# Optimization experiments

Hardware: AMD Instinct MI355X
Metric: run time of the kernel (lower is better)

The kernel has to match this reference:

```python
import jax, jax.numpy as jnp
import numpy as np

V, H, E = 32000, 512, 256
B, NC, LSC, LCM, LIS = 64, 10, 128, 64, 32


def _lstm_last(x, Wih, Whh, b):
    # x: [N, T, E] -> final (h, c) each [N, H]. PyTorch gate order i, f, g, o.
    N = x.shape[0]
    Hd = Whh.shape[1]
    h0 = jnp.zeros((N, Hd), x.dtype)

    def step(carry, xt):
        h, c = carry
        z = xt @ Wih.T + h @ Whh.T + b  # [N, 4H]
        i, f, g, o = jnp.split(z, 4, axis=-1)
        c = jax.nn.sigmoid(f) * c + jax.nn.sigmoid(i) * jnp.tanh(g)
        h = jax.nn.sigmoid(o) * jnp.tanh(c)
        return (h, c), None

    (h, c), _ = jax.lax.scan(step, (h0, h0), jnp.swapaxes(x, 0, 1))
    return h, c


def setup_inputs() -> dict:
    key = jax.random.key(0)
    ks = jax.random.split(key, 24)
    s = 0.02
    inp = {
        'comments': jax.random.randint(ks[0], (B, NC, LSC), 0, V),
        'cm': jax.random.randint(ks[1], (B, NC, LCM), 0, V),
        'issue': jax.random.randint(ks[2], (B, LIS), 0, V),
        'emb_sc': jax.random.normal(ks[3], (V, E), jnp.float32) * s,
        'emb_cm': jax.random.normal(ks[4], (V, E), jnp.float32) * s,
        'emb_is': jax.random.normal(ks[5], (V, E), jnp.float32) * s,
        'Wih_sc': jax.random.normal(ks[6], (4 * H, E), jnp.float32) * s,
        'Whh_sc': jax.random.normal(ks[7], (4 * H, H), jnp.float32) * s,
        'b_sc': jnp.zeros((4 * H,), jnp.float32),
        'Wih_cm': jax.random.normal(ks[8], (4 * H, E), jnp.float32) * s,
        'Whh_cm': jax.random.normal(ks[9], (4 * H, H), jnp.float32) * s,
        'b_cm': jnp.zeros((4 * H,), jnp.float32),
        'Wih_is': jax.random.normal(ks[10], (4 * H, E), jnp.float32) * s,
        'Whh_is': jax.random.normal(ks[11], (4 * H, H), jnp.float32) * s,
        'b_is': jnp.zeros((4 * H,), jnp.float32),
        'Wmh': jax.random.normal(ks[12], (1, 2 * H), jnp.float32) * s,
        'bmh': jnp.zeros((1,), jnp.float32),
        'Wmc': jax.random.normal(ks[13], (1, 2 * H), jnp.float32) * s,
        'bmc': jnp.zeros((1,), jnp.float32),
        'Wfh': jax.random.normal(ks[14], (H, NC + H), jnp.float32) * s,
        'bfh': jnp.zeros((H,), jnp.float32),
        'Wfc': jax.random.normal(ks[15], (H, NC + H), jnp.float32) * s,
        'bfc': jnp.zeros((H,), jnp.float32),
    }
    return inp


def reference(comments, cm, issue, emb_sc, emb_cm, emb_is,
              Wih_sc, Whh_sc, b_sc, Wih_cm, Whh_cm, b_cm,
              Wih_is, Whh_is, b_is, Wmh, bmh, Wmc, bmc,
              Wfh, bfh, Wfc, bfc):
    Bb, Nc, Lsc = comments.shape
    sc_ids = comments.reshape(Bb * Nc, Lsc)
    cm_ids = cm.reshape(Bb * Nc, cm.shape[-1])
    # embed + LSTM over all B*NC commit sequences at once (batched ragged loop)
    h_sc, c_sc = _lstm_last(emb_sc[sc_ids], Wih_sc, Whh_sc, b_sc)
    h_cm, c_cm = _lstm_last(emb_cm[cm_ids], Wih_cm, Whh_cm, b_cm)
    hcat = jnp.concatenate([h_sc, h_cm], axis=-1)  # [B*NC, 2H]
    ccat = jnp.concatenate([c_sc, c_cm], axis=-1)
    hm = (hcat @ Wmh.T + bmh).reshape(Bb, Nc)  # per-commit scalar merge
    cmm = (ccat @ Wmc.T + bmc).reshape(Bb, Nc)
    h_is, c_is = _lstm_last(emb_is[issue], Wih_is, Whh_is, b_is)  # [B, H]
    h = jnp.concatenate([hm, h_is], axis=-1) @ Wfh.T + bfh  # [B, H]
    c = jnp.concatenate([cmm, c_is], axis=-1) @ Wfc.T + bfc
    # torch code cats per-PR (1,1,H) states along dim=1 -> (1, B, H)
    return h[None], c[None]
```

## Files before the change

### kernel.cpp

```cpp
#include <hip/hip_runtime.h>
#include <math.h>

#define E 256
#define Hh 512

typedef __attribute__((ext_vector_type(8))) short short8;
typedef __attribute__((ext_vector_type(4))) float f32x4;
typedef __attribute__((ext_vector_type(4))) unsigned uint4v;


struct LstmP {
  const int* ids;
  const float* emb;
  const unsigned short* Wih;
  const unsigned short* Whh;
  const float* bias;
  unsigned short* h0;
  float* c;
  int T;
  int nh;
};

__device__ unsigned g_cnt[42*32];

__device__ __forceinline__ float bf2f(unsigned short x){
  union { unsigned u; float f; } v; v.u = ((unsigned)x) << 16; return v.f;
}
__device__ __forceinline__ unsigned short f2bf(float f){
  union { float f; unsigned u; } v; v.f = f;
  unsigned u = v.u;
  return (unsigned short)((u + 0x7fffu + ((u >> 16) & 1u)) >> 16);
}
__device__ __forceinline__ short8 cvt8(const float* p){
  f32x4 x = *(const f32x4*)p;
  f32x4 y = *(const f32x4*)(p + 4);
  short8 r;
  r[0]=(short)f2bf(x[0]); r[1]=(short)f2bf(x[1]); r[2]=(short)f2bf(x[2]); r[3]=(short)f2bf(x[3]);
  r[4]=(short)f2bf(y[0]); r[5]=(short)f2bf(y[1]); r[6]=(short)f2bf(y[2]); r[7]=(short)f2bf(y[3]);
  return r;
}
__device__ __forceinline__ float sigm(float x){
  return __builtin_amdgcn_rcpf(1.0f + __builtin_amdgcn_exp2f(-1.44269504f*x));
}
__device__ __forceinline__ float tanh_f(float x){
  return 1.0f - 2.0f*__builtin_amdgcn_rcpf(1.0f + __builtin_amdgcn_exp2f(2.88539008f*x));
}

__global__ void zero_ws_kernel(uint4* p, int n){
  int i = blockIdx.x*256 + threadIdx.x;
  if (i < n){ uint4 z; z.x=0u; z.y=0u; z.z=0u; z.w=0u; p[i]=z; }
}

__global__ void zero_cnt_kernel(){
  for (int i = threadIdx.x; i < 42*32; i += 256) g_cnt[i] = 0u;
}

__global__ __launch_bounds__(256) void cvt_kernel(const float* src, unsigned short* dst, int n8){
  int i = blockIdx.x*256 + threadIdx.x;
  if (i < n8){
    *(short8*)(dst + (size_t)i*8) = cvt8(src + (size_t)i*8);
  }
}

__global__ __launch_bounds__(256, 2) void lstm_persist(LstmP sc, LstmP cm, LstmP is_)
{
  __shared__ unsigned short hs[32][512];
  __shared__ unsigned short sh_h[32][72];

  LstmP P; int tile, grp;
  {
    int idx = blockIdx.x;
    if (idx < 160){ P = sc;  tile = idx;        grp = tile >> 3; }
    else if (idx < 320){ P = cm;  tile = idx - 160;  grp = 20 + (tile >> 3); }
    else { P = is_; tile = idx - 320;  grp = 40 + (tile >> 3); }
  }
  const int tid  = threadIdx.x;
  const int w    = tid >> 6;
  const int lane = tid & 63;
  const int l15  = lane & 15;
  const int q    = lane >> 4;
  const int mb = tile >> 3, jt = tile & 7;
  const int m0 = mb*32, j0 = jt*64;
  const int jw = j0 + w*16;
  const int T = P.T;
  unsigned* cgp = &g_cnt[grp*32];
  const int xr = (l15 & 7) << 3;

  const int* idrow[2];
  #pragma unroll
  for (int mi=0; mi<2; ++mi){
    int m = m0 + mi*16 + l15;
    idrow[mi] = P.ids + (size_t)m*T;
  }
  const unsigned short* bg1[4];
  const unsigned short* bg2[4];
  float bvv[4];
  #pragma unroll
  for (int g=0; g<4; ++g){
    int n = g*Hh + jw + l15;
    bg1[g] = P.Wih + (size_t)n*E  + q*8;
    bg2[g] = P.Whh + (size_t)n*Hh + q*8;
    bvv[g] = P.bias[n];
  }

  float cc[8];
  #pragma unroll
  for (int i=0;i<8;++i) cc[i] = 0.f;

  for (int t = 0; t < T; ++t){
    const unsigned short* h_in  = P.h0 + (size_t)(t&1)*P.nh;
    unsigned short*       h_out = P.h0 + (size_t)((t+1)&1)*P.nh;

    f32x4 acc[2][4];
    #pragma unroll
    for (int i=0;i<2;++i)
      #pragma unroll
      for (int g=0;g<4;++g) acc[i][g] = (f32x4){0.f,0.f,0.f,0.f};

    uint4v stg[8];
    if (t > 0){
      if (tid == 0){
        unsigned tgt = 8u * (unsigned)t;
        long guard = 0;
        while (__hip_atomic_load(cgp, __ATOMIC_RELAXED, __HIP_MEMORY_SCOPE_AGENT) < tgt){
          __builtin_amdgcn_s_sleep(1);
          if (++guard > 2000000L) break;
        }
      }
      __syncthreads();
      asm volatile("" ::: "memory");

      const unsigned short* base = h_in + (size_t)m0*Hh;
      #pragma unroll
      for (int i=0;i<8;++i){
        int d = (tid + 256*i + (jt<<8)) & 2047;
        const void* ap = (const void*)(base + (size_t)d*8);
        asm volatile("global_load_dwordx4 %0, %1, off sc0 sc1"
                     : "=v"(stg[i]) : "v"(ap) : "memory");
      }
    }

    const float* ap1[2];
    #pragma unroll
    for (int mi=0; mi<2; ++mi){
      int id = idrow[mi][t];
      ap1[mi] = P.emb + (size_t)id*E + q*8;
    }
    #pragma unroll 2
    for (int kc=0; kc<8; ++kc){
      short8 a[2], b[4];
      #pragma unroll
      for (int mi=0;mi<2;++mi) a[mi] = cvt8(ap1[mi] + kc*32);
      #pragma unroll
      for (int g=0;g<4;++g) b[g] = *(const short8*)(bg1[g] + kc*32);
      #pragma unroll
      for (int mi=0;mi<2;++mi)
        #pragma unroll
        for (int g=0;g<4;++g)
          acc[mi][g] = __builtin_amdgcn_mfma_f32_16x16x32_bf16(a[mi], b[g], acc[mi][g], 0,0,0);
    }

    if (t > 0){
      asm volatile("s_waitcnt vmcnt(0)" ::: "memory");
      #pragma unroll
      for (int i=0;i<8;++i){
        int d = (tid + 256*i + (jt<<8)) & 2047;
        int row = d >> 6, cp = d & 63;
        *(uint4v*)&hs[row][(cp ^ (row & 7)) << 3] = stg[i];
      }
      __syncthreads();

      #pragma unroll 2
      for (int kc=0; kc<16; ++kc){
        short8 a[2], b[4];
        #pragma unroll
        for (int mi=0;mi<2;++mi)
          a[mi] = *(const short8*)&hs[mi*16 + l15][(kc*32 + q*8) ^ xr];
        #pragma unroll
        for (int g=0;g<4;++g) b[g] = *(const short8*)(bg2[g] + kc*32);
        #pragma unroll
        for (int mi=0;mi<2;++mi)
          #pragma unroll
          for (int g=0;g<4;++g)
            acc[mi][g] = __builtin_amdgcn_mfma_f32_16x16x32_bf16(a[mi], b[g], acc[mi][g], 0,0,0);
      }
    }

    #pragma unroll
    for (int mi=0;mi<2;++mi)
      #pragma unroll
      for (int r=0;r<4;++r){
        float zi = acc[mi][0][r] + bvv[0];
        float zf = acc[mi][1][r] + bvv[1];
        float zg = acc[mi][2][r] + bvv[2];
        float zo = acc[mi][3][r] + bvv[3];
        float cn = sigm(zf)*cc[mi*4+r] + sigm(zi)*tanh_f(zg);
        float hn = sigm(zo)*tanh_f(cn);
        cc[mi*4+r] = cn;
        sh_h[mi*16 + q*4 + r][w*16 + l15] = f2bf(hn);
      }
    __syncthreads();

    {
      int m = tid >> 3, oct = tid & 7;
      uint4v pk = *(const uint4v*)&sh_h[m][oct*8];
      void* ap = (void*)(h_out + (size_t)(m0+m)*Hh + j0 + oct*8);
      asm volatile("global_store_dwordx4 %0, %1, off sc0 sc1"
                   :: "v"(ap), "v"(pk) : "memory");
    }

    asm volatile("s_waitcnt vmcnt(0)" ::: "memory");
    __syncthreads();
    if (tid == 0)
      __hip_atomic_fetch_add(cgp, 1u, __ATOMIC_RELAXED, __HIP_MEMORY_SCOPE_AGENT);
  }

  #pragma unroll
  for (int mi=0;mi<2;++mi)
    #pragma unroll
    for (int r=0;r<4;++r)
      P.c[(size_t)(m0 + mi*16 + q*4 + r)*Hh + jw + l15] = cc[mi*4+r];
}

__global__ __launch_bounds__(256) void out_kernel(
    const unsigned short* hsc, const unsigned short* hcm, const unsigned short* his,
    const float* csc, const float* ccm, const float* cis,
    const float* Wmh, const float* bmh, const float* Wmc, const float* bmc,
    const float* Wfh, const float* bfh, const float* Wfc, const float* bfc,
    float* out)
{
  const int b    = blockIdx.x >> 2;
  const int kind = (blockIdx.x >> 1) & 1;
  const int half = blockIdx.x & 1;
  const int tid  = threadIdx.x;
  const int w = tid >> 6, lane = tid & 63;
  const float* Wm = kind ? Wmc : Wmh;
  const float* bm = kind ? bmc : bmh;
  const float* Wf = kind ? Wfc : Wfh;
  const float* bf = kind ? bfc : bfh;

  __shared__ float vis[512];
  __shared__ float wred[10][4];
  __shared__ float hmb[10];

  for (int k = tid; k < 512; k += 256)
    vis[k] = kind ? cis[(size_t)b*512 + k] : bf2f(his[(size_t)b*512 + k]);

  float pn[10];
  #pragma unroll
  for (int nc=0; nc<10; ++nc){
    size_t n = (size_t)b*10 + nc;
    float a = 0.f;
    #pragma unroll
    for (int kk=0; kk<2; ++kk){
      int k = tid + kk*256;
      float v1 = kind ? csc[n*512+k] : bf2f(hsc[n*512+k]);
      float v2 = kind ? ccm[n*512+k] : bf2f(hcm[n*512+k]);
      a += Wm[k]*v1 + Wm[512+k]*v2;
    }
    pn[nc] = a;
  }
  #pragma unroll
  for (int nc=0; nc<10; ++nc){
    float v = pn[nc];
    #pragma unroll
    for (int off=32; off; off>>=1) v += __shfl_down(v, off);
    if (lane == 0) wred[nc][w] = v;
  }
  __syncthreads();
  if (tid < 10) hmb[tid] = wred[tid][0] + wred[tid][1] + wred[tid][2] + wred[tid][3] + bm[0];
  __syncthreads();

  const int u = tid + 256*half;
  const float* wr = Wf + (size_t)u*522;
  float a0 = bf[u], a1 = 0.f, a2 = 0.f, a3 = 0.f;
  #pragma unroll
  for (int k=0; k<10; ++k) a0 += wr[k]*hmb[k];
  #pragma unroll 4
  for (int k=0; k<512; k+=4){
    a0 += wr[10+k] * vis[k];
    a1 += wr[11+k] * vis[k+1];
    a2 += wr[12+k] * vis[k+2];
    a3 += wr[13+k] * vis[k+3];
  }
  out[(size_t)kind*32768 + (size_t)b*512 + u] = (a0+a1) + (a2+a3);
}

extern "C" void kernel_launch(void* const* d_in, const int* in_sizes, int n_in,
                              void* d_out, int out_size, void* d_ws, size_t ws_size,
                              hipStream_t stream) {
  const int* comments = (const int*)d_in[0];
  const int* cm_ids   = (const int*)d_in[1];
  const int* issue    = (const int*)d_in[2];
  const float* emb_sc = (const float*)d_in[3];
  const float* emb_cm = (const float*)d_in[4];
  const float* emb_is = (const float*)d_in[5];
  const float* Wih_sc = (const float*)d_in[6];
  const float* Whh_sc = (const float*)d_in[7];
  const float* b_sc   = (const float*)d_in[8];
  const float* Wih_cm = (const float*)d_in[9];
  const float* Whh_cm = (const float*)d_in[10];
  const float* b_cm   = (const float*)d_in[11];
  const float* Wih_is = (const float*)d_in[12];
  const float* Whh_is = (const float*)d_in[13];
  const float* b_is   = (const float*)d_in[14];
  const float* Wmh = (const float*)d_in[15];
  const float* bmh = (const float*)d_in[16];
  const float* Wmc = (const float*)d_in[17];
  const float* bmc = (const float*)d_in[18];
  const float* Wfh = (const float*)d_in[19];
  const float* bfh = (const float*)d_in[20];
  const float* Wfc = (const float*)d_in[21];
  const float* bfc = (const float*)d_in[22];

  char* p = (char*)d_ws;
  unsigned short* hb_sc = (unsigned short*)p; p += (size_t)2*640*512*2;
  unsigned short* hb_cm = (unsigned short*)p; p += (size_t)2*640*512*2;
  unsigned short* hb_is = (unsigned short*)p; p += (size_t)2*64*512*2;
  float* c_sc = (float*)p; p += (size_t)640*512*4;
  float* c_cm = (float*)p; p += (size_t)640*512*4;
  float* c_is = (float*)p; p += (size_t)64*512*4;
  size_t zero_bytes = (size_t)(p - (char*)d_ws);
  unsigned short* Wih_sc_b = (unsigned short*)p; p += (size_t)2048*256*2;
  unsigned short* Whh_sc_b = (unsigned short*)p; p += (size_t)2048*512*2;
  unsigned short* Wih_cm_b = (unsigned short*)p; p += (size_t)2048*256*2;
  unsigned short* Whh_cm_b = (unsigned short*)p; p += (size_t)2048*512*2;
  unsigned short* Wih_is_b = (unsigned short*)p; p += (size_t)2048*256*2;
  unsigned short* Whh_is_b = (unsigned short*)p; p += (size_t)2048*512*2;

  int n4 = (int)(zero_bytes/16);
  zero_ws_kernel<<<(n4+255)/256, 256, 0, stream>>>((uint4*)d_ws, n4);
  zero_cnt_kernel<<<1, 256, 0, stream>>>();

  const int nih8 = 2048*256/8, nhh8 = 2048*512/8;
  cvt_kernel<<<(nih8+255)/256, 256, 0, stream>>>(Wih_sc, Wih_sc_b, nih8);
  cvt_kernel<<<(nhh8+255)/256, 256, 0, stream>>>(Whh_sc, Whh_sc_b, nhh8);
  cvt_kernel<<<(nih8+255)/256, 256, 0, stream>>>(Wih_cm, Wih_cm_b, nih8);
  cvt_kernel<<<(nhh8+255)/256, 256, 0, stream>>>(Whh_cm, Whh_cm_b, nhh8);
  cvt_kernel<<<(nih8+255)/256, 256, 0, stream>>>(Wih_is, Wih_is_b, nih8);
  cvt_kernel<<<(nhh8+255)/256, 256, 0, stream>>>(Whh_is, Whh_is_b, nhh8);

  LstmP Psc = { comments, emb_sc, Wih_sc_b, Whh_sc_b, b_sc, hb_sc, c_sc, 128, 640*512 };
  LstmP Pcm = { cm_ids,   emb_cm, Wih_cm_b, Whh_cm_b, b_cm, hb_cm, c_cm,  64, 640*512 };
  LstmP Pis = { issue,    emb_is, Wih_is_b, Whh_is_b, b_is, hb_is, c_is,  32,  64*512 };
  lstm_persist<<<336, 256, 0, stream>>>(Psc, Pcm, Pis);

  out_kernel<<<256, 256, 0, stream>>>(hb_sc, hb_cm, hb_is, c_sc, c_cm, c_is,
                                      Wmh, bmh, Wmc, bmc, Wfh, bfh, Wfc, bfc,
                                      (float*)d_out);
}
```

Before: 3.125 ms.

## Widen LSTM tiles to 128 hidden columns and pre-convert embeddings to bf16

Each persistent block now computes a 32x128 hidden slice instead of 32x64, halving the grid to 168 blocks and the number of blocks per sync group from 8 to 4. Each block loads the shared h tile once and reuses it across twice as many weight columns, which cuts redundant global h reads and counter waits. Separately, if the workspace is large enough, the three embedding tables are converted to bf16 up front so the per-step gather skips the fp32-to-bf16 conversion. The costs are more accumulator registers per thread, fewer blocks to spread work across CUs, and three full-table conversion passes over 32000x256 rows on every call.

```diff
diff --git a/kernel.cpp b/kernel.cpp
--- a/kernel.cpp
+++ b/kernel.cpp
@@ -12,6 +12,7 @@
 struct LstmP {
   const int* ids;
   const float* emb;
+  const unsigned short* embb;
   const unsigned short* Wih;
   const unsigned short* Whh;
   const float* bias;
@@ -62,26 +63,27 @@
   }
 }
 
+template<int EBF>
 __global__ __launch_bounds__(256, 2) void lstm_persist(LstmP sc, LstmP cm, LstmP is_)
 {
   __shared__ unsigned short hs[32][512];
-  __shared__ unsigned short sh_h[32][72];
+  __shared__ unsigned short sh_h[32][136];
 
   LstmP P; int tile, grp;
   {
     int idx = blockIdx.x;
-    if (idx < 160){ P = sc;  tile = idx;        grp = tile >> 3; }
-    else if (idx < 320){ P = cm;  tile = idx - 160;  grp = 20 + (tile >> 3); }
-    else { P = is_; tile = idx - 320;  grp = 40 + (tile >> 3); }
+    if (idx < 80){ P = sc;  tile = idx;        grp = tile >> 2; }
+    else if (idx < 160){ P = cm;  tile = idx - 80;   grp = 20 + (tile >> 2); }
+    else { P = is_; tile = idx - 160;  grp = 40 + (tile >> 2); }
   }
   const int tid  = threadIdx.x;
   const int w    = tid >> 6;
   const int lane = tid & 63;
   const int l15  = lane & 15;
   const int q    = lane >> 4;
-  const int mb = tile >> 3, jt = tile & 7;
-  const int m0 = mb*32, j0 = jt*64;
-  const int jw = j0 + w*16;
+  const int mb = tile >> 2, jt = tile & 3;
+  const int m0 = mb*32, j0 = jt*128;
+  const int jw = j0 + w*32;
   const int T = P.T;
   unsigned* cgp = &g_cnt[grp*32];
   const int xr = (l15 & 7) << 3;
@@ -94,33 +96,36 @@
   }
   const unsigned short* bg1[4];
   const unsigned short* bg2[4];
-  float bvv[4];
+  float bvv[4][2];
   #pragma unroll
   for (int g=0; g<4; ++g){
     int n = g*Hh + jw + l15;
     bg1[g] = P.Wih + (size_t)n*E  + q*8;
     bg2[g] = P.Whh + (size_t)n*Hh + q*8;
-    bvv[g] = P.bias[n];
-  }
-
-  float cc[8];
-  #pragma unroll
-  for (int i=0;i<8;++i) cc[i] = 0.f;
+    bvv[g][0] = P.bias[n];
+    bvv[g][1] = P.bias[n + 16];
+  }
+
+  float cc[16];
+  #pragma unroll
+  for (int i=0;i<16;++i) cc[i] = 0.f;
 
   for (int t = 0; t < T; ++t){
     const unsigned short* h_in  = P.h0 + (size_t)(t&1)*P.nh;
     unsigned short*       h_out = P.h0 + (size_t)((t+1)&1)*P.nh;
 
-    f32x4 acc[2][4];
+    f32x4 acc[2][4][2];
     #pragma unroll
     for (int i=0;i<2;++i)
       #pragma unroll
-      for (int g=0;g<4;++g) acc[i][g] = (f32x4){0.f,0.f,0.f,0.f};
+      for (int g=0;g<4;++g)
+        #pragma unroll
+        for (int ni=0;ni<2;++ni) acc[i][g][ni] = (f32x4){0.f,0.f,0.f,0.f};
 
     uint4v stg[8];
     if (t > 0){
       if (tid == 0){
-        unsigned tgt = 8u * (unsigned)t;
+        unsigned tgt = 4u * (unsigned)t;
         long guard = 0;
         while (__hip_atomic_load(cgp, __ATOMIC_RELAXED, __HIP_MEMORY_SCOPE_AGENT) < tgt){
           __builtin_amdgcn_s_sleep(1);
@@ -133,38 +138,48 @@
       const unsigned short* base = h_in + (size_t)m0*Hh;
       #pragma unroll
       for (int i=0;i<8;++i){
-        int d = (tid + 256*i + (jt<<8)) & 2047;
+        int d = (tid + 256*i + (jt<<9)) & 2047;
         const void* ap = (const void*)(base + (size_t)d*8);
         asm volatile("global_load_dwordx4 %0, %1, off sc0 sc1"
                      : "=v"(stg[i]) : "v"(ap) : "memory");
       }
     }
 
-    const float* ap1[2];
+    const unsigned short* ap1b[2];
+    const float* ap1f[2];
     #pragma unroll
     for (int mi=0; mi<2; ++mi){
       int id = idrow[mi][t];
-      ap1[mi] = P.emb + (size_t)id*E + q*8;
+      if (EBF) ap1b[mi] = P.embb + (size_t)id*E + q*8;
+      else     ap1f[mi] = P.emb  + (size_t)id*E + q*8;
     }
     #pragma unroll 2
     for (int kc=0; kc<8; ++kc){
-      short8 a[2], b[4];
-      #pragma unroll
-      for (int mi=0;mi<2;++mi) a[mi] = cvt8(ap1[mi] + kc*32);
-      #pragma unroll
-      for (int g=0;g<4;++g) b[g] = *(const short8*)(bg1[g] + kc*32);
+      short8 a[2], b[4][2];
+      #pragma unroll
+      for (int mi=0;mi<2;++mi){
+        if (EBF) a[mi] = *(const short8*)(ap1b[mi] + kc*32);
+        else     a[mi] = cvt8(ap1f[mi] + kc*32);
+      }
+      #pragma unroll
+      for (int g=0;g<4;++g)
+        #pragma unroll
+        for (int ni=0;ni<2;++ni)
+          b[g][ni] = *(const short8*)(bg1[g] + ni*16*E + kc*32);
       #pragma unroll
       for (int mi=0;mi<2;++mi)
         #pragma unroll
         for (int g=0;g<4;++g)
-          acc[mi][g] = __builtin_amdgcn_mfma_f32_16x16x32_bf16(a[mi], b[g], acc[mi][g], 0,0,0);
+          #pragma unroll
+          for (int ni=0;ni<2;++ni)
+            acc[mi][g][ni] = __builtin_amdgcn_mfma_f32_16x16x32_bf16(a[mi], b[g][ni], acc[mi][g][ni], 0,0,0);
     }
 
     if (t > 0){
       asm volatile("s_waitcnt vmcnt(0)" ::: "memory");
       #pragma unroll
       for (int i=0;i<8;++i){
-        int d = (tid + 256*i + (jt<<8)) & 2047;
+        int d = (tid + 256*i + (jt<<9)) & 2047;
         int row = d >> 6, cp = d & 63;
         *(uint4v*)&hs[row][(cp ^ (row & 7)) << 3] = stg[i];
       }
@@ -172,37 +187,46 @@
 
       #pragma unroll 2
       for (int kc=0; kc<16; ++kc){
-        short8 a[2], b[4];
+        short8 a[2], b[4][2];
         #pragma unroll
         for (int mi=0;mi<2;++mi)
           a[mi] = *(const short8*)&hs[mi*16 + l15][(kc*32 + q*8) ^ xr];
         #pragma unroll
-        for (int g=0;g<4;++g) b[g] = *(const short8*)(bg2[g] + kc*32);
+        for (int g=0;g<4;++g)
+          #pragma unroll
+          for (int ni=0;ni<2;++ni)
+            b[g][ni] = *(const short8*)(bg2[g] + ni*16*Hh + kc*32);
         #pragma unroll
         for (int mi=0;mi<2;++mi)
           #pragma unroll
           for (int g=0;g<4;++g)
-            acc[mi][g] = __builtin_amdgcn_mfma_f32_16x16x32_bf16(a[mi], b[g], acc[mi][g], 0,0,0);
+            #pragma unroll
+            for (int ni=0;ni<2;++ni)
+              acc[mi][g][ni] = __builtin_amdgcn_mfma_f32_16x16x32_bf16(a[mi], b[g][ni], acc[mi][g][ni], 0,0,0);
       }
     }
 
     #pragma unroll
     for (int mi=0;mi<2;++mi)
       #pragma unroll
-      for (int r=0;r<4;++r){
-        float zi = acc[mi][0][r] + bvv[0];
-        float zf = acc[mi][1][r] + bvv[1];
-        float zg = acc[mi][2][r] + bvv[2];
-        float zo = acc[mi][3][r] + bvv[3];
-        float cn = sigm(zf)*cc[mi*4+r] + sigm(zi)*tanh_f(zg);
-        float hn = sigm(zo)*tanh_f(cn);
-        cc[mi*4+r] = cn;
-        sh_h[mi*16 + q*4 + r][w*16 + l15] = f2bf(hn);
-      }
+      for (int ni=0;ni<2;++ni)
+        #pragma unroll
+        for (int r=0;r<4;++r){
+          float zi = acc[mi][0][ni][r] + bvv[0][ni];
+          float zf = acc[mi][1][ni][r] + bvv[1][ni];
+          float zg = acc[mi][2][ni][r] + bvv[2][ni];
+          float zo = acc[mi][3][ni][r] + bvv[3][ni];
+          float cn = sigm(zf)*cc[mi*8+ni*4+r] + sigm(zi)*tanh_f(zg);
+          float hn = sigm(zo)*tanh_f(cn);
+          cc[mi*8+ni*4+r] = cn;
+          sh_h[mi*16 + q*4 + r][w*32 + ni*16 + l15] = f2bf(hn);
+        }
     __syncthreads();
 
-    {
-      int m = tid >> 3, oct = tid & 7;
+    #pragma unroll
+    for (int i=0;i<2;++i){
+      int idx = tid + 256*i;
+      int m = idx >> 4, oct = idx & 15;
       uint4v pk = *(const uint4v*)&sh_h[m][oct*8];
       void* ap = (void*)(h_out + (size_t)(m0+m)*Hh + j0 + oct*8);
       asm volatile("global_store_dwordx4 %0, %1, off sc0 sc1"
@@ -218,8 +242,10 @@
   #pragma unroll
   for (int mi=0;mi<2;++mi)
     #pragma unroll
-    for (int r=0;r<4;++r)
-      P.c[(size_t)(m0 + mi*16 + q*4 + r)*Hh + jw + l15] = cc[mi*4+r];
+    for (int ni=0;ni<2;++ni)
+      #pragma unroll
+      for (int r=0;r<4;++r)
+        P.c[(size_t)(m0 + mi*16 + q*4 + r)*Hh + jw + ni*16 + l15] = cc[mi*8+ni*4+r];
 }
 
 __global__ __launch_bounds__(256) void out_kernel(
@@ -327,6 +353,12 @@
   unsigned short* Whh_cm_b = (unsigned short*)p; p += (size_t)2048*512*2;
   unsigned short* Wih_is_b = (unsigned short*)p; p += (size_t)2048*256*2;
   unsigned short* Whh_is_b = (unsigned short*)p; p += (size_t)2048*512*2;
+  const size_t emb_elems = (size_t)32000*256;
+  unsigned short* emb_sc_b = (unsigned short*)p; p += emb_elems*2;
+  unsigned short* emb_cm_b = (unsigned short*)p; p += emb_elems*2;
+  unsigned short* emb_is_b = (unsigned short*)p; p += emb_elems*2;
+  size_t need_bf = (size_t)(p - (char*)d_ws);
+  const bool ebf = (ws_size >= need_bf);
 
   int n4 = (int)(zero_bytes/16);
   zero_ws_kernel<<<(n4+255)/256, 256, 0, stream>>>((uint4*)d_ws, n4);
@@ -339,11 +371,18 @@
   cvt_kernel<<<(nhh8+255)/256, 256, 0, stream>>>(Whh_cm, Whh_cm_b, nhh8);
   cvt_kernel<<<(nih8+255)/256, 256, 0, stream>>>(Wih_is, Wih_is_b, nih8);
   cvt_kernel<<<(nhh8+255)/256, 256, 0, stream>>>(Whh_is, Whh_is_b, nhh8);
-
-  LstmP Psc = { comments, emb_sc, Wih_sc_b, Whh_sc_b, b_sc, hb_sc, c_sc, 128, 640*512 };
-  LstmP Pcm = { cm_ids,   emb_cm, Wih_cm_b, Whh_cm_b, b_cm, hb_cm, c_cm,  64, 640*512 };
-  LstmP Pis = { issue,    emb_is, Wih_is_b, Whh_is_b, b_is, hb_is, c_is,  32,  64*512 };
-  lstm_persist<<<336, 256, 0, stream>>>(Psc, Pcm, Pis);
+  if (ebf){
+    const int ne8 = (int)(emb_elems/8);
+    cvt_kernel<<<(ne8+255)/256, 256, 0, stream>>>(emb_sc, emb_sc_b, ne8);
+    cvt_kernel<<<(ne8+255)/256, 256, 0, stream>>>(emb_cm, emb_cm_b, ne8);
+    cvt_kernel<<<(ne8+255)/256, 256, 0, stream>>>(emb_is, emb_is_b, ne8);
+  }
+
+  LstmP Psc = { comments, emb_sc, emb_sc_b, Wih_sc_b, Whh_sc_b, b_sc, hb_sc, c_sc, 128, 640*512 };
+  LstmP Pcm = { cm_ids,   emb_cm, emb_cm_b, Wih_cm_b, Whh_cm_b, b_cm, hb_cm, c_cm,  64, 640*512 };
+  LstmP Pis = { issue,    emb_is, emb_is_b, Wih_is_b, Whh_is_b, b_is, hb_is, c_is,  32,  64*512 };
+  if (ebf) lstm_persist<1><<<168, 256, 0, stream>>>(Psc, Pcm, Pis);
+  else     lstm_persist<0><<<168, 256, 0, stream>>>(Psc, Pcm, Pis);
 
   out_kernel<<<256, 256, 0, stream>>>(hb_sc, hb_cm, hb_is, c_sc, c_cm, c_is,
                                       Wmh, bmh, Wmc, bmc, Wfh, bfh, Wfc, bfc,
```

Result: slower. 3.693 ms (+18.1%).

## Use 64-row LSTM tiles, keep Whh in registers, pre-convert embeddings to bf16

Applied to the files above, without the earlier changes.

The persistent LSTM kernel now gives each block 64 batch rows instead of 32, halving the grid to 168 blocks at one block per CU. Each block's Whh slice is loaded once into registers instead of being re-read from memory every timestep. The hidden-state gather is split into two halves so it overlaps with the input-projection MFMAs. When the workspace is large enough, the three embedding tables are converted to bf16 up front, so the inner loop skips the per-step fp32-to-bf16 conversion. The cost is very high register pressure, fewer blocks in flight, and an extra pass over large tables for the embedding conversion.

```diff
diff --git a/kernel.cpp b/kernel.cpp
--- a/kernel.cpp
+++ b/kernel.cpp
@@ -12,6 +12,7 @@
 struct LstmP {
   const int* ids;
   const float* emb;
+  const unsigned short* embb;
   const unsigned short* Wih;
   const unsigned short* Whh;
   const float* bias;
@@ -62,17 +63,18 @@
   }
 }
 
-__global__ __launch_bounds__(256, 2) void lstm_persist(LstmP sc, LstmP cm, LstmP is_)
+template<int EBF>
+__global__ __launch_bounds__(256, 1) void lstm_persist(LstmP sc, LstmP cm, LstmP is_)
 {
-  __shared__ unsigned short hs[32][512];
-  __shared__ unsigned short sh_h[32][72];
+  __shared__ unsigned short hs[64][512];
+  __shared__ unsigned short sh_h[64][72];
 
   LstmP P; int tile, grp;
   {
     int idx = blockIdx.x;
-    if (idx < 160){ P = sc;  tile = idx;        grp = tile >> 3; }
-    else if (idx < 320){ P = cm;  tile = idx - 160;  grp = 20 + (tile >> 3); }
-    else { P = is_; tile = idx - 320;  grp = 40 + (tile >> 3); }
+    if (idx < 80){ P = sc;  tile = idx;        grp = tile >> 3; }
+    else if (idx < 160){ P = cm;  tile = idx - 80;   grp = 20 + (tile >> 3); }
+    else { P = is_; tile = idx - 160;  grp = 40 + (tile >> 3); }
   }
   const int tid  = threadIdx.x;
   const int w    = tid >> 6;
@@ -80,44 +82,50 @@
   const int l15  = lane & 15;
   const int q    = lane >> 4;
   const int mb = tile >> 3, jt = tile & 7;
-  const int m0 = mb*32, j0 = jt*64;
+  const int m0 = mb*64, j0 = jt*64;
   const int jw = j0 + w*16;
   const int T = P.T;
   unsigned* cgp = &g_cnt[grp*32];
   const int xr = (l15 & 7) << 3;
 
-  const int* idrow[2];
-  #pragma unroll
-  for (int mi=0; mi<2; ++mi){
+  const int* idrow[4];
+  #pragma unroll
+  for (int mi=0; mi<4; ++mi){
     int m = m0 + mi*16 + l15;
     idrow[mi] = P.ids + (size_t)m*T;
   }
   const unsigned short* bg1[4];
-  const unsigned short* bg2[4];
   float bvv[4];
   #pragma unroll
   for (int g=0; g<4; ++g){
     int n = g*Hh + jw + l15;
-    bg1[g] = P.Wih + (size_t)n*E  + q*8;
-    bg2[g] = P.Whh + (size_t)n*Hh + q*8;
+    bg1[g] = P.Wih + (size_t)n*E + q*8;
     bvv[g] = P.bias[n];
   }
 
-  float cc[8];
-  #pragma unroll
-  for (int i=0;i<8;++i) cc[i] = 0.f;
+  short8 wb[16][4];
+  #pragma unroll
+  for (int g=0; g<4; ++g){
+    const unsigned short* bp = P.Whh + (size_t)(g*Hh + jw + l15)*Hh + q*8;
+    #pragma unroll
+    for (int kc=0; kc<16; ++kc)
+      wb[kc][g] = *(const short8*)(bp + kc*32);
+  }
+
+  float cc[16];
+  #pragma unroll
+  for (int i=0;i<16;++i) cc[i] = 0.f;
 
   for (int t = 0; t < T; ++t){
     const unsigned short* h_in  = P.h0 + (size_t)(t&1)*P.nh;
     unsigned short*       h_out = P.h0 + (size_t)((t+1)&1)*P.nh;
 
-    f32x4 acc[2][4];
-    #pragma unroll
-    for (int i=0;i<2;++i)
+    f32x4 acc[4][4];
+    #pragma unroll
+    for (int i=0;i<4;++i)
       #pragma unroll
       for (int g=0;g<4;++g) acc[i][g] = (f32x4){0.f,0.f,0.f,0.f};
 
-    uint4v stg[8];
     if (t > 0){
       if (tid == 0){
         unsigned tgt = 8u * (unsigned)t;
@@ -129,65 +137,76 @@
       }
       __syncthreads();
       asm volatile("" ::: "memory");
-
-      const unsigned short* base = h_in + (size_t)m0*Hh;
+    }
+
+    const unsigned short* ap1b[4];
+    const float* ap1f[4];
+    #pragma unroll
+    for (int mi=0; mi<4; ++mi){
+      int id = idrow[mi][t];
+      if (EBF) ap1b[mi] = P.embb + (size_t)id*E + q*8;
+      else     ap1f[mi] = P.emb  + (size_t)id*E + q*8;
+    }
+
+    const unsigned short* base = h_in + (size_t)m0*Hh;
+    #pragma unroll
+    for (int half=0; half<2; ++half){
+      uint4v stg[8];
+      if (t > 0){
+        #pragma unroll
+        for (int i=0;i<8;++i){
+          int d = (tid + 256*(i + 8*half) + (jt<<9)) & 4095;
+          const void* ap = (const void*)(base + (size_t)d*8);
+          asm volatile("global_load_dwordx4 %0, %1, off sc0 sc1"
+                       : "=v"(stg[i]) : "v"(ap) : "memory");
+        }
+      }
       #pragma unroll
-      for (int i=0;i<8;++i){
-        int d = (tid + 256*i + (jt<<8)) & 2047;
-        const void* ap = (const void*)(base + (size_t)d*8);
-        asm volatile("global_load_dwordx4 %0, %1, off sc0 sc1"
-                     : "=v"(stg[i]) : "v"(ap) : "memory");
-      }
-    }
-
-    const float* ap1[2];
-    #pragma unroll
-    for (int mi=0; mi<2; ++mi){
-      int id = idrow[mi][t];
-      ap1[mi] = P.emb + (size_t)id*E + q*8;
-    }
-    #pragma unroll 2
-    for (int kc=0; kc<8; ++kc){
-      short8 a[2], b[4];
-      #pragma unroll
-      for (int mi=0;mi<2;++mi) a[mi] = cvt8(ap1[mi] + kc*32);
-      #pragma unroll
-      for (int g=0;g<4;++g) b[g] = *(const short8*)(bg1[g] + kc*32);
-      #pragma unroll
-      for (int mi=0;mi<2;++mi)
-        #pragma unroll
-        for (int g=0;g<4;++g)
-          acc[mi][g] = __builtin_amdgcn_mfma_f32_16x16x32_bf16(a[mi], b[g], acc[mi][g], 0,0,0);
-    }
-
-    if (t > 0){
-      asm volatile("s_waitcnt vmcnt(0)" ::: "memory");
-      #pragma unroll
-      for (int i=0;i<8;++i){
-        int d = (tid + 256*i + (jt<<8)) & 2047;
-        int row = d >> 6, cp = d & 63;
-        *(uint4v*)&hs[row][(cp ^ (row & 7)) << 3] = stg[i];
-      }
-      __syncthreads();
-
-      #pragma unroll 2
-      for (int kc=0; kc<16; ++kc){
-        short8 a[2], b[4];
-        #pragma unroll
-        for (int mi=0;mi<2;++mi)
-          a[mi] = *(const short8*)&hs[mi*16 + l15][(kc*32 + q*8) ^ xr];
-        #pragma unroll
-        for (int g=0;g<4;++g) b[g] = *(const short8*)(bg2[g] + kc*32);
-        #pragma unroll
-        for (int mi=0;mi<2;++mi)
+      for (int kk=0; kk<4; ++kk){
+        int kc = half*4 + kk;
+        short8 a[4], b[4];
+        #pragma unroll
+        for (int mi=0;mi<4;++mi){
+          if (EBF) a[mi] = *(const short8*)(ap1b[mi] + kc*32);
+          else     a[mi] = cvt8(ap1f[mi] + kc*32);
+        }
+        #pragma unroll
+        for (int g=0;g<4;++g) b[g] = *(const short8*)(bg1[g] + kc*32);
+        #pragma unroll
+        for (int mi=0;mi<4;++mi)
           #pragma unroll
           for (int g=0;g<4;++g)
             acc[mi][g] = __builtin_amdgcn_mfma_f32_16x16x32_bf16(a[mi], b[g], acc[mi][g], 0,0,0);
       }
-    }
-
-    #pragma unroll
-    for (int mi=0;mi<2;++mi)
+      if (t > 0){
+        asm volatile("s_waitcnt vmcnt(0)" ::: "memory");
+        #pragma unroll
+        for (int i=0;i<8;++i){
+          int d = (tid + 256*(i + 8*half) + (jt<<9)) & 4095;
+          int row = d >> 6, cp = d & 63;
+          *(uint4v*)&hs[row][(cp ^ (row & 7)) << 3] = stg[i];
+        }
+      }
+    }
+
+    if (t > 0){
+      __syncthreads();
+      #pragma unroll
+      for (int kc=0; kc<16; ++kc){
+        short8 a[4];
+        #pragma unroll
+        for (int mi=0;mi<4;++mi)
+          a[mi] = *(const short8*)&hs[mi*16 + l15][(kc*32 + q*8) ^ xr];
+        #pragma unroll
+        for (int mi=0;mi<4;++mi)
+          #pragma unroll
+          for (int g=0;g<4;++g)
+            acc[mi][g] = __builtin_amdgcn_mfma_f32_16x16x32_bf16(a[mi], wb[kc][g], acc[mi][g], 0,0,0);
+      }
+    }
+
+    #pragma unroll
+    for (int mi=0;mi<4;++mi)
       #pragma unroll
       for (int r=0;r<4;++r){
         float zi = acc[mi][0][r] + bvv[0];
@@ -201,8 +220,10 @@
       }
     __syncthreads();
 
-    {
-      int m = tid >> 3, oct = tid & 7;
+    #pragma unroll
+    for (int i=0;i<2;++i){
+      int idx = tid + 256*i;
+      int m = idx >> 3, oct = idx & 7;
       uint4v pk = *(const uint4v*)&sh_h[m][oct*8];
       void* ap = (void*)(h_out + (size_t)(m0+m)*Hh + j0 + oct*8);
       asm volatile("global_store_dwordx4 %0, %1, off sc0 sc1"
@@ -216,7 +237,7 @@
   }
 
   #pragma unroll
-  for (int mi=0;mi<2;++mi)
+  for (int mi=0;mi<4;++mi)
     #pragma unroll
     for (int r=0;r<4;++r)
       P.c[(size_t)(m0 + mi*16 + q*4 + r)*Hh + jw + l15] = cc[mi*4+r];
@@ -327,6 +348,12 @@
   unsigned short* Whh_cm_b = (unsigned short*)p; p += (size_t)2048*512*2;
   unsigned short* Wih_is_b = (unsigned short*)p; p += (size_t)2048*256*2;
   unsigned short* Whh_is_b = (unsigned short*)p; p += (size_t)2048*512*2;
+  const size_t emb_elems = (size_t)32000*256;
+  unsigned short* emb_sc_b = (unsigned short*)p; p += emb_elems*2;
+  unsigned short* emb_cm_b = (unsigned short*)p; p += emb_elems*2;
+  unsigned short* emb_is_b = (unsigned short*)p; p += emb_elems*2;
+  size_t need_bf = (size_t)(p - (char*)d_ws);
+  const bool ebf = (ws_size >= need_bf);
 
   int n4 = (int)(zero_bytes/16);
   zero_ws_kernel<<<(n4+255)/256, 256, 0, stream>>>((uint4*)d_ws, n4);
@@ -339,11 +366,18 @@
   cvt_kernel<<<(nhh8+255)/256, 256, 0, stream>>>(Whh_cm, Whh_cm_b, nhh8);
   cvt_kernel<<<(nih8+255)/256, 256, 0, stream>>>(Wih_is, Wih_is_b, nih8);
   cvt_kernel<<<(nhh8+255)/256, 256, 0, stream>>>(Whh_is, Whh_is_b, nhh8);
-
-  LstmP Psc = { comments, emb_sc, Wih_sc_b, Whh_sc_b, b_sc, hb_sc, c_sc, 128, 640*512 };
-  LstmP Pcm = { cm_ids,   emb_cm, Wih_cm_b, Whh_cm_b, b_cm, hb_cm, c_cm,  64, 640*512 };
-  LstmP Pis = { issue,    emb_is, Wih_is_b, Whh_is_b, b_is, hb_is, c_is,  32,  64*512 };
-  lstm_persist<<<336, 256, 0, stream>>>(Psc, Pcm, Pis);
+  if (ebf){
+    const int ne8 = (int)(emb_elems/8);
+    cvt_kernel<<<(ne8+255)/256, 256, 0, stream>>>(emb_sc, emb_sc_b, ne8);
+    cvt_kernel<<<(ne8+255)/256, 256, 0, stream>>>(emb_cm, emb_cm_b, ne8);
+    cvt_kernel<<<(ne8+255)/256, 256, 0, stream>>>(emb_is, emb_is_b, ne8);
+  }
+
+  LstmP Psc = { comments, emb_sc, emb_sc_b, Wih_sc_b, Whh_sc_b, b_sc, hb_sc, c_sc, 128, 640*512 };
+  LstmP Pcm = { cm_ids,   emb_cm, emb_cm_b, Wih_cm_b, Whh_cm_b, b_cm, hb_cm, c_cm,  64, 640*512 };
+  LstmP Pis = { issue,    emb_is, emb_is_b, Wih_is_b, Whh_is_b, b_is, hb_is, c_is,  32,  64*512 };
+  if (ebf) lstm_persist<1><<<168, 256, 0, stream>>>(Psc, Pcm, Pis);
+  else     lstm_persist<0><<<168, 256, 0, stream>>>(Psc, Pcm, Pis);
 
   out_kernel<<<256, 256, 0, stream>>>(hb_sc, hb_cm, hb_is, c_sc, c_cm, c_is,
                                       Wmh, bmh, Wmc, bmc, Wfh, bfh, Wfc, bfc,
```

New measurement: 2.650 ms. -15.2%, faster.
